# Kernel optimization log

Measured on AMD Instinct MI355X. Metric: run time of the kernel, lower is better.

## Reference

```python
import jax, jax.numpy as jnp
import numpy as np

B_T = 32      # input capsule types
C_T = 32      # output capsule types
K = 3         # conv kernel
STRIDE = 2
H = 4         # pose matrix side
HH = H * H
ITERS = 3
EPS = 1e-10
LN_2PI = np.float32(np.log(2.0 * np.pi))


def setup_inputs() -> dict:
    key = jax.random.key(0)
    k1, k2, k3, k4, k5 = jax.random.split(key, 5)
    b, win = 16, 14
    poses = jax.random.normal(k1, (b, HH * B_T, win, win), dtype=jnp.float32)
    activations = jax.random.uniform(k2, (b, B_T, win, win), dtype=jnp.float32)
    W = jax.random.normal(k3, (B_T, K, K, C_T, H, H), dtype=jnp.float32)
    beta_v = jax.random.normal(k4, (1, C_T, 1, 1), dtype=jnp.float32)
    beta_a = jax.random.normal(k5, (1, C_T, 1), dtype=jnp.float32)
    lambda_ = jnp.float32(0.01)
    return {"lambda_": lambda_, "poses": poses, "activations": activations,
            "W": W, "beta_v": beta_v, "beta_a": beta_a}


def _em_routing(lambda_, a_in, V, beta_v, beta_a, b, Bkk, Cww, ww):
    sg = jax.lax.stop_gradient
    R = jnp.full((b, Bkk, Cww), 1.0 / C_T, dtype=V.dtype)
    a = mu = None
    for i in range(ITERS):
        R4 = (R * a_in)[..., None]                       # (b,Bkk,Cww,1)
        sum_R = R4.sum(1)                                # (b,Cww,1)
        mu = ((R4 * V).sum(1) / sum_R)[:, None]          # (b,1,Cww,hh)
        sigma_sq = ((R4 * (V - mu) ** 2).sum(1) / sum_R)[:, None]
        cost = (beta_v + jnp.log(jnp.sqrt(sigma_sq).reshape(b, C_T, ww, HH) + EPS)) \
               * sum_R.reshape(b, C_T, ww, 1)            # (b,C,ww,hh)
        a = jax.nn.sigmoid(lambda_ * (beta_a - cost.sum(-1)))  # (b,C,ww)
        a = a.reshape(b, Cww)
        if i != ITERS - 1:
            Vd, mud, ssd = sg(V), sg(mu), sg(sigma_sq)
            ln_p = -(Vd - mud) ** 2 / (2.0 * ssd) - jnp.log(jnp.sqrt(ssd)) - 0.5 * LN_2PI
            p = jnp.exp(ln_p)                            # (b,Bkk,Cww,hh)
            ap = sg(a)[:, None, :] * p.sum(-1)           # (b,Bkk,Cww)
            R = sg(ap / (ap.sum(2, keepdims=True) + EPS) + EPS)
    return a, mu


def _forward(lambda_, poses, activations, W, beta_v, beta_a):
    b, win = poses.shape[0], poses.shape[2]
    w = (win - K) // STRIDE + 1
    ww = w * w
    Bkk = K * K * B_T
    Cww = ww * C_T
    pose = poses.reshape(b, HH, B_T, win, win).transpose(0, 2, 3, 4, 1)
    # patch extraction indices: row ri[i, ki] = stride*i + ki
    ri = (STRIDE * np.arange(w))[:, None] + np.arange(K)  # (w, K)
    P = pose[:, :, ri]
    P = P[:, :, :, :, ri]         # (b,B,w_i,K_i,w_j,K_j,hh)
    # stack order in torch: dim=-1 index = j*w + i, patch dims (K_i,K_j,hh)
    patches = P.transpose(0, 1, 3, 5, 6, 4, 2).reshape(b, B_T, K, K, HH, ww)
    # faithful to torch .view (row-major reinterpretation mixing hh and ww)
    poses_r = patches.reshape(b, B_T, K, K, 1, w, w, H, H)
    W_hat = W[None, :, :, :, :, None, None, :, :]          # (1,B,K,K,C,1,1,h,h)
    votes = jnp.matmul(W_hat, poses_r)                     # (b,B,K,K,C,w,w,h,h)
    # activation patches, same (j*w+i) ordering
    A = activations[:, :, ri]
    A = A[:, :, :, :, ri]         # (b,B,w_i,K_i,w_j,K_j)
    act_p = A.transpose(0, 1, 3, 5, 4, 2).reshape(b, B_T, K, K, ww)
    a_ = jnp.broadcast_to(act_p.reshape(b, Bkk, 1, ww), (b, Bkk, C_T, ww)).reshape(b, Bkk, Cww)
    V = votes.reshape(b, Bkk, Cww, HH)
    a, mu = _em_routing(lambda_, a_, V, beta_v, beta_a, b, Bkk, Cww, ww)
    return mu.reshape(b, C_T, w, w, HH), a.reshape(b, C_T, w, w)


def reference(lambda_, poses, activations, W, beta_v, beta_a):
    return _forward(lambda_, poses, activations, W, beta_v, beta_a)
```

## Files before the change

### kernel.cpp

```cpp
#include <hip/hip_runtime.h>

#define EPS 1e-10f
#define HALF_LN2PI 0.91893853320467274f
#define LOG2E 1.4426950408889634f


__device__ __forceinline__ float fexp2(float x) {
    float r;
    asm("v_exp_f32 %0, %1" : "=v"(r) : "v"(x));
    return r;
}

template <int IT>
__global__ __launch_bounds__(128)
void m_pass(const float* __restrict__ poses, const float* __restrict__ acts,
            float* __restrict__ Ptg, float* __restrict__ actp,
            const float* __restrict__ W,
            const float* __restrict__ ap_buf, const float* __restrict__ denom_prev,
            float* __restrict__ Mpart)
{
    __shared__ __align__(16) float Pt_lds[1152];
    __shared__ float act_lds[72];
    __shared__ float invd_lds[72];
    __shared__ __align__(16) float red[1152];

    const int tid  = threadIdx.x;
    const int wave = tid >> 6, lane = tid & 63;
    const int cl   = lane >> 2;
    const int bid  = blockIdx.x;
    const int blk  = bid >> 2, iq = bid & 3;
    const int bb   = blk / 36, p = blk - bb * 36;
    const int i0   = iq * 72;
    const size_t pbase  = (size_t)blk * 4608;
    const size_t apbase = (size_t)blk * 9216;

    if (IT == 0) {
        const int base = (p / 6) * 96 + (p % 6) * 16;
        for (int e = tid; e < 1152; e += 128) {
            int il = e >> 4, j = e & 15;
            int i = i0 + il;
            int hc = j >> 2, m = j & 3;
            int f = base + m * 4 + hc;
            int h = f / 36, sp = f - h * 36;
            int y = sp / 6, x = sp - y * 6;
            int B = i / 9, kk = i - B * 9;
            int ki = kk / 3, kj = kk - ki * 3;
            float v = poses[(size_t)((bb * 512 + h * 32 + B) * 14 + 2 * x + ki) * 14 + 2 * y + kj];
            Pt_lds[e] = v;
            Ptg[pbase + (size_t)i0 * 16 + e] = v;
        }
        const int y = p / 6, x = p - y * 6;
        for (int e = tid; e < 72; e += 128) {
            int i = i0 + e;
            int B = i / 9, kk = i - B * 9;
            int ki = kk / 3, kj = kk - ki * 3;
            float v = acts[(size_t)((bb * 32 + B) * 14 + 2 * x + ki) * 14 + 2 * y + kj];
            act_lds[e] = v;
            actp[blk * 288 + i] = v;
        }
    } else {
        const float4* src = (const float4*)(Ptg + pbase + (size_t)i0 * 16);
        float4* dst = (float4*)Pt_lds;
        for (int e = tid; e < 288; e += 128) dst[e] = src[e];
        for (int e = tid; e < 72; e += 128) {
            act_lds[e]  = actp[blk * 288 + i0 + e];
            invd_lds[e] = 1.0f / (denom_prev[bb * 288 + i0 + e] + EPS);
        }
    }
    __syncthreads();

    float acc[18];
#pragma unroll
    for (int k = 0; k < 18; ++k) acc[k] = 0.f;

    const float* Wt  = W + (size_t)(i0 + wave * 36) * 512 + (lane << 2);
    const float* apc = ap_buf + apbase + (size_t)(i0 + wave * 36) * 32 + cl;

#pragma unroll 6
    for (int t = 0; t < 36; ++t) {
        const int il = wave * 36 + t;
        const float4 wva = *(const float4*)(Wt + (size_t)t * 512);
        const float4 wvb = *(const float4*)(Wt + (size_t)t * 512 + 256);
        float Ra, Rb;
        if (IT == 0) {
            Ra = 1.0f / 32.0f; Rb = 1.0f / 32.0f;
        } else {
            const float inv = invd_lds[il];
            Ra = fmaf(apc[(size_t)t * 32],      inv, EPS);
            Rb = fmaf(apc[(size_t)t * 32 + 16], inv, EPS);
        }
        const float a_in = act_lds[il];
        const float R4a = Ra * a_in, R4b = Rb * a_in;
        acc[16] += R4a; acc[17] += R4b;
#pragma unroll
        for (int hc = 0; hc < 4; ++hc) {
            const float4 pv = *(const float4*)&Pt_lds[il * 16 + hc * 4];
            float Va = wva.x * pv.x + wva.y * pv.y + wva.z * pv.z + wva.w * pv.w;
            float Vb = wvb.x * pv.x + wvb.y * pv.y + wvb.z * pv.z + wvb.w * pv.w;
            acc[hc]      = fmaf(R4a, Va, acc[hc]);
            acc[4 + hc]  = fmaf(R4a * Va, Va, acc[4 + hc]);
            acc[8 + hc]  = fmaf(R4b, Vb, acc[8 + hc]);
            acc[12 + hc] = fmaf(R4b * Vb, Vb, acc[12 + hc]);
        }
    }

    if (wave == 1) {
#pragma unroll
        for (int k = 0; k < 18; ++k) red[lane * 18 + k] = acc[k];
    }
    __syncthreads();
    if (wave == 0) {
        float* mp = Mpart + (size_t)bid * 1152;
#pragma unroll
        for (int k = 0; k < 18; ++k)
            mp[k * 64 + lane] = acc[k] + red[lane * 18 + k];
    }
}

template <int FINAL>
__global__ __launch_bounds__(64)
void f_pass(float* __restrict__ Mpart, const float* __restrict__ beta_v,
            const float* __restrict__ beta_a, const float* __restrict__ lambda_p,
            float* __restrict__ d_out)
{
    const int lane = threadIdx.x;
    const int cl = lane >> 2, hr = lane & 3;
    const int blk = blockIdx.x;
    const int bb = blk / 36, p = blk - bb * 36;
    float* mp = Mpart + (size_t)blk * 4608;

    float s[18];
#pragma unroll
    for (int k = 0; k < 18; ++k)
        s[k] = mp[k * 64 + lane] + mp[1152 + k * 64 + lane]
             + mp[2304 + k * 64 + lane] + mp[3456 + k * 64 + lane];

    const float lam = lambda_p[0];
    float muv[8], n2v[8], hlv[8], av[2];
#pragma unroll
    for (int q = 0; q < 2; ++q) {
        const int c = cl + q * 16;
        const float sR = s[16 + q];
        float ls = 0.f;
#pragma unroll
        for (int hc = 0; hc < 4; ++hc) {
            const float S1 = s[q * 8 + hc];
            const float S2 = s[q * 8 + 4 + hc];
            const float mu = S1 / sR;
            float ss = S2 / sR - mu * mu;
            ss = fmaxf(ss, 1e-30f);
            muv[q * 4 + hc] = mu;
            n2v[q * 4 + hc] = (-0.5f / ss) * LOG2E;
            hlv[q * 4 + hc] = (-0.5f * __logf(ss) - HALF_LN2PI) * LOG2E;
            ls += __logf(sqrtf(ss) + EPS);
        }
        ls += __shfl_xor(ls, 1);
        ls += __shfl_xor(ls, 2);
        const float cost = sR * (16.0f * beta_v[c] + ls);
        av[q] = 1.0f / (1.0f + __expf(-lam * (beta_a[c] - cost)));
    }

    if (FINAL) {
#pragma unroll
        for (int q = 0; q < 2; ++q) {
            const int c = cl + q * 16;
#pragma unroll
            for (int hc = 0; hc < 4; ++hc)
                d_out[(size_t)bb * 18432 + (size_t)(c * 36 + p) * 16 + hr * 4 + hc] = muv[q * 4 + hc];
            if (hr == 0)
                d_out[294912 + (size_t)bb * 1152 + c * 36 + p] = av[q];
        }
    } else {
        asm volatile("s_waitcnt vmcnt(0)" ::: "memory");
#pragma unroll
        for (int q = 0; q < 2; ++q) {
#pragma unroll
            for (int hc = 0; hc < 4; ++hc) {
                const int ix = lane * 4 + q * 256 + hc;
                mp[ix]        = muv[q * 4 + hc];
                mp[512 + ix]  = n2v[q * 4 + hc];
                mp[1024 + ix] = hlv[q * 4 + hc];
            }
            if (hr == 0) mp[1536 + cl + q * 16] = av[q];
        }
    }
}

__global__ __launch_bounds__(128, 5)
void e_pass(const float* __restrict__ Ptg, const float* __restrict__ Mpart,
            const float* __restrict__ W,
            float* __restrict__ ap_buf, float* __restrict__ denom_next)
{
    __shared__ __align__(16) float Pt_lds[1152];

    const int tid  = threadIdx.x;
    const int wave = tid >> 6, lane = tid & 63;
    const int cl   = lane >> 2, hr = lane & 3;
    const int bid  = blockIdx.x;
    const int blk  = bid >> 2, iq = bid & 3;
    const int bb   = blk / 36;
    const int i0   = iq * 72;
    const size_t pbase  = (size_t)blk * 4608;
    const size_t apbase = (size_t)blk * 9216;

    {
        const float4* src = (const float4*)(Ptg + pbase + (size_t)i0 * 16);
        float4* dst = (float4*)Pt_lds;
        for (int e = tid; e < 288; e += 128) dst[e] = src[e];
    }

    const float* st = Mpart + (size_t)blk * 4608;
    __align__(16) float mua[4], mub[4], na[4], nb[4], ha[4], hb[4];
    *(float4*)mua = *(const float4*)&st[lane * 4];
    *(float4*)mub = *(const float4*)&st[lane * 4 + 256];
    *(float4*)na  = *(const float4*)&st[512 + lane * 4];
    *(float4*)nb  = *(const float4*)&st[512 + lane * 4 + 256];
    *(float4*)ha  = *(const float4*)&st[1024 + lane * 4];
    *(float4*)hb  = *(const float4*)&st[1024 + lane * 4 + 256];
    const float aca = st[1536 + cl], acb = st[1536 + cl + 16];
    __syncthreads();

    const float* Wt  = W + (size_t)(i0 + wave * 36) * 512 + (lane << 2);
    float* apw       = ap_buf + apbase + (size_t)(i0 + wave * 36) * 32 + cl;
    float* dnx       = denom_next + bb * 288 + i0 + wave * 36;

#pragma unroll
    for (int t = 0; t < 36; ++t) {
        const int il = wave * 36 + t;
        const float4 wva = *(const float4*)(Wt + (size_t)t * 512);
        const float4 wvb = *(const float4*)(Wt + (size_t)t * 512 + 256);
        float pea = 0.f, peb = 0.f;
#pragma unroll
        for (int hc = 0; hc < 4; ++hc) {
            const float4 pv = *(const float4*)&Pt_lds[il * 16 + hc * 4];
            float Va = wva.x * pv.x + wva.y * pv.y + wva.z * pv.z + wva.w * pv.w;
            float Vb = wvb.x * pv.x + wvb.y * pv.y + wvb.z * pv.z + wvb.w * pv.w;
            float da = Va - mua[hc];
            float db = Vb - mub[hc];
            pea += fexp2(fmaf(da * da, na[hc], ha[hc]));
            peb += fexp2(fmaf(db * db, nb[hc], hb[hc]));
        }
        pea += __shfl_xor(pea, 1);
        pea += __shfl_xor(pea, 2);
        peb += __shfl_xor(peb, 1);
        peb += __shfl_xor(peb, 2);
        const float apa = aca * pea;
        const float apb = acb * peb;
        if (hr == 0) {
            apw[(size_t)t * 32]      = apa;
            apw[(size_t)t * 32 + 16] = apb;
        }
        float dsum = apa + apb;
        dsum += __shfl_xor(dsum, 4);
        dsum += __shfl_xor(dsum, 8);
        dsum += __shfl_xor(dsum, 16);
        dsum += __shfl_xor(dsum, 32);
        if (lane == 0)
            atomicAdd(&dnx[t], dsum);
    }
}

extern "C" void kernel_launch(void* const* d_in, const int* in_sizes, int n_in,
                              void* d_out, int out_size, void* d_ws, size_t ws_size,
                              hipStream_t stream)
{
    const float* lambda_p = (const float*)d_in[0];
    const float* poses    = (const float*)d_in[1];
    const float* acts     = (const float*)d_in[2];
    const float* W        = (const float*)d_in[3];
    const float* beta_v   = (const float*)d_in[4];
    const float* beta_a   = (const float*)d_in[5];
    float* out = (float*)d_out;

    float* ws     = (float*)d_ws;
    float* Ptg    = ws;
    float* actp   = Ptg + 2654208;
    float* ap_buf = actp + 165888;
    float* Mpart  = ap_buf + 5308416;
    float* denom0 = Mpart + 2654208;
    float* denom1 = denom0 + 4608;

    hipMemsetAsync(denom0, 0, 2 * 4608 * sizeof(float), stream);
    m_pass<0><<<2304, 128, 0, stream>>>(poses, acts, Ptg, actp, W, ap_buf, denom1, Mpart);
    f_pass<0><<<576, 64, 0, stream>>>(Mpart, beta_v, beta_a, lambda_p, out);
    e_pass<<<2304, 128, 0, stream>>>(Ptg, Mpart, W, ap_buf, denom0);
    m_pass<1><<<2304, 128, 0, stream>>>(poses, acts, Ptg, actp, W, ap_buf, denom0, Mpart);
    f_pass<0><<<576, 64, 0, stream>>>(Mpart, beta_v, beta_a, lambda_p, out);
    e_pass<<<2304, 128, 0, stream>>>(Ptg, Mpart, W, ap_buf, denom1);
    m_pass<2><<<2304, 128, 0, stream>>>(poses, acts, Ptg, actp, W, ap_buf, denom1, Mpart);
    f_pass<1><<<576, 64, 0, stream>>>(Mpart, beta_v, beta_a, lambda_p, out);
}
```

Baseline: 192.9 us.

## Stage e_pass ap results in LDS and reduce denominators per block

Each e_pass iteration now writes its ap values into a shared-memory tile instead of storing scattered scalars to global memory and running a 4-step shuffle reduction plus an atomic. After the loop, the tile is copied to global memory with coalesced float4 stores, and 72 threads each sum a row with a skewed index to avoid bank conflicts before issuing one atomic per row. The launch-bounds occupancy hint is removed and the loop is only partially unrolled, which changes register pressure. The extra 9 KB of LDS per block may lower occupancy.

```diff
diff --git a/kernel.cpp b/kernel.cpp
--- a/kernel.cpp
+++ b/kernel.cpp
@@ -186,12 +186,13 @@
     }
 }
 
-__global__ __launch_bounds__(128, 5)
+__global__ __launch_bounds__(128)
 void e_pass(const float* __restrict__ Ptg, const float* __restrict__ Mpart,
             const float* __restrict__ W,
             float* __restrict__ ap_buf, float* __restrict__ denom_next)
 {
     __shared__ __align__(16) float Pt_lds[1152];
+    __shared__ __align__(16) float ap_lds[2304];
 
     const int tid  = threadIdx.x;
     const int wave = tid >> 6, lane = tid & 63;
@@ -220,11 +221,9 @@
     const float aca = st[1536 + cl], acb = st[1536 + cl + 16];
     __syncthreads();
 
-    const float* Wt  = W + (size_t)(i0 + wave * 36) * 512 + (lane << 2);
-    float* apw       = ap_buf + apbase + (size_t)(i0 + wave * 36) * 32 + cl;
-    float* dnx       = denom_next + bb * 288 + i0 + wave * 36;
-
-#pragma unroll
+    const float* Wt = W + (size_t)(i0 + wave * 36) * 512 + (lane << 2);
+
+#pragma unroll 6
     for (int t = 0; t < 36; ++t) {
         const int il = wave * 36 + t;
         const float4 wva = *(const float4*)(Wt + (size_t)t * 512);
@@ -244,19 +243,24 @@
         pea += __shfl_xor(pea, 2);
         peb += __shfl_xor(peb, 1);
         peb += __shfl_xor(peb, 2);
-        const float apa = aca * pea;
-        const float apb = acb * peb;
         if (hr == 0) {
-            apw[(size_t)t * 32]      = apa;
-            apw[(size_t)t * 32 + 16] = apb;
-        }
-        float dsum = apa + apb;
-        dsum += __shfl_xor(dsum, 4);
-        dsum += __shfl_xor(dsum, 8);
-        dsum += __shfl_xor(dsum, 16);
-        dsum += __shfl_xor(dsum, 32);
-        if (lane == 0)
-            atomicAdd(&dnx[t], dsum);
+            ap_lds[il * 32 + cl]      = aca * pea;
+            ap_lds[il * 32 + cl + 16] = acb * peb;
+        }
+    }
+    __syncthreads();
+
+    {
+        const float4* s4 = (const float4*)ap_lds;
+        float4* d4 = (float4*)(ap_buf + apbase + (size_t)i0 * 32);
+        for (int e = tid; e < 576; e += 128) d4[e] = s4[e];
+    }
+    if (tid < 72) {
+        float s = 0.f;
+#pragma unroll
+        for (int c = 0; c < 32; ++c)
+            s += ap_lds[tid * 32 + ((c + tid) & 31)];
+        atomicAdd(&denom_next[bb * 288 + i0 + tid], s);
     }
 }
 
```

Result: faster. 184.2 us (-4.5%).
